# Optimization experiments

Measured on AMD Instinct MI355X. Metric: run time of the kernel, lower is better.

Reference implementation:

```python
import jax, jax.numpy as jnp
import numpy as np

IMG = 64
N = IMG * IMG          # 4096, spatial tokens = LayerNorm dim
F2 = 128 * 128         # 16384, feature_size**2 = Mlp input dim
B, C = 8, 512
EPS = 1e-5
LOG_MAX = float(np.log(1.0 / 0.01))  # clamp max for logit_scale


def setup_inputs() -> dict:
    key = jax.random.key(0)
    ks = jax.random.split(key, 8)
    s1 = 1.0 / np.sqrt(F2)
    s2 = 1.0 / np.sqrt(N)
    return {
        "x": jax.random.normal(ks[0], (B, C, N), jnp.float32),
        "feature": jax.random.normal(ks[1], (B, C, F2), jnp.float32),
        "fc1_w": jax.random.uniform(ks[2], (N, F2), jnp.float32, -s1, s1),
        "fc1_b": jax.random.uniform(ks[3], (N,), jnp.float32, -s1, s1),
        "fc2_w": jax.random.uniform(ks[4], (N, N), jnp.float32, -s2, s2),
        "fc2_b": jax.random.uniform(ks[5], (N,), jnp.float32, -s2, s2),
        "logit_scale": jnp.full((1, 1, N), np.log(10.0), jnp.float32),
        "norm_w": jnp.ones((N,), jnp.float32),
        "norm_b": jnp.zeros((N,), jnp.float32),
    }


def reference(x, feature, fc1_w, fc1_b, fc2_w, fc2_b, logit_scale, norm_w, norm_b):
    # Mlp: (B,C,F2) -> (B,C,N), ReLU activation, drop=0
    h = jax.nn.relu(jnp.einsum('bcf,nf->bcn', feature, fc1_w) + fc1_b)
    feat = jnp.einsum('bch,nh->bcn', h, fc2_w) + fc2_b        # (B,C,N)
    feat = jnp.swapaxes(feat, 1, 2)                            # (B,N,C)
    scale = jnp.exp(jnp.minimum(logit_scale, LOG_MAX))         # (1,1,N)
    temp = jnp.einsum('bnc,bcm->bnm', feat, x) * scale         # (B,N,N)
    temp = jax.nn.softmax(temp, axis=1)                        # softmax over dim=1
    out = jnp.einsum('bcn,bnm->bcm', x, temp)                  # (B,C,N)
    # LayerNorm over last dim
    mu = jnp.mean(out, axis=-1, keepdims=True)
    var = jnp.var(out, axis=-1, keepdims=True)
    out = (out - mu) * jax.lax.rsqrt(var + EPS) * norm_w + norm_b
    return out
```

## Files before the change

### kernel.cpp

```cpp
#include <hip/hip_runtime.h>
#include <stdint.h>

using u16 = unsigned short;
typedef unsigned int u32;
typedef __attribute__((ext_vector_type(4))) float f32x4;
typedef __attribute__((ext_vector_type(8))) short short8;

typedef const __attribute__((address_space(1))) u32* gas_ptr;
typedef __attribute__((address_space(3))) u32* las_ptr;

__device__ __forceinline__ u16 f2bf_u(float f) {
    u32 u = __builtin_bit_cast(u32, f);
    u32 r = 0x7fffu + ((u >> 16) & 1u);
    return (u16)((u + r) >> 16);
}
__device__ __forceinline__ float bfu2f(u16 h) {
    u32 u = ((u32)h) << 16;
    return __builtin_bit_cast(float, u);
}
__device__ __forceinline__ void split2(float v, u16& hi, u16& lo) {
    hi = f2bf_u(v);
    lo = f2bf_u(v - bfu2f(hi));
}

__device__ __forceinline__ void gload16(const void* g, void* l) {
    __builtin_amdgcn_global_load_lds((gas_ptr)g, (las_ptr)l, 16, 0, 0);
}


#define STAGE(CBUF, KT)                                                      \
  {                                                                          \
    const int kk_ = (KT) << 5;                                               \
    _Pragma("unroll")                                                        \
    for (int it_ = 0; it_ < 2; ++it_) {                                      \
      const int rb_ = it_ * 128 + w * 16;                                    \
      const int lo_ = (CBUF) * 8192 + rb_ * 32;                              \
      const size_t ga_ = (size_t)(brow + rb_ + srow) * lda + (kk_ + sca);    \
      const size_t gb_ = (size_t)(bcol + rb_ + srow) * lda + (kk_ + sca);    \
      gload16(A0 + ga_, &As0[lo_]);                                          \
      gload16(B0 + gb_, &Bs0[lo_]);                                          \
      if constexpr (SPLIT) gload16(A1 + ga_, &As1[lo_]);                     \
    }                                                                        \
  }

#define BLOQ(Q, KT)                                                          \
  {                                                                          \
    const u16* bb_ = B1 + (size_t)(bcol + wc * 64 + lr) * lda                \
                     + (((KT) << 5) + ((l >> 4) * 8));                       \
    _Pragma("unroll")                                                        \
    for (int n_ = 0; n_ < 4; ++n_)                                           \
      Q[n_] = *(const short8*)(bb_ + (size_t)(n_ * 16) * lda);               \
  }

#define AREAD(DSTH, DSTL, I)                                                 \
  {                                                                          \
    const int ro_ = cbv_ * 8192 +                                            \
        (lrw + (((I) >> 2) * 64 + ((I) & 3) * 16)) * 32 + cr;                \
    DSTH = *(const short8*)&As0[ro_];                                        \
    if constexpr (SPLIT) DSTL = *(const short8*)&As1[ro_];                   \
  }

#define PHASE(KT, CB, Q)                                                     \
  {                                                                          \
    const int cbv_ = (CB);                                                   \
    if ((KT) == NT - 1) {                                                    \
      asm volatile("s_waitcnt vmcnt(0)" ::: "memory");                       \
    } else {                                                                 \
      if constexpr (SPLIT) asm volatile("s_waitcnt vmcnt(10)" ::: "memory"); \
      else asm volatile("s_waitcnt vmcnt(4)" ::: "memory");                  \
    }                                                                        \
    __builtin_amdgcn_s_barrier();                                            \
    __builtin_amdgcn_sched_barrier(0);                                       \
    {                                                                        \
      int cs_ = cbv_ + 2; if (cs_ >= 3) cs_ -= 3;                            \
      if ((KT) + 2 < NT) STAGE(cs_, (KT) + 2);                               \
    }                                                                        \
    short8 bh_[4];                                                           \
    _Pragma("unroll")                                                        \
    for (int n_ = 0; n_ < 4; ++n_)                                           \
      bh_[n_] = *(const short8*)&Bs0[cbv_ * 8192 +                           \
                                     (wc * 64 + n_ * 16 + lr) * 32 + cr];    \
    short8 ah_[2][2], al_[2][2];                                             \
    AREAD(ah_[0][0], al_[0][0], 0);                                          \
    AREAD(ah_[0][1], al_[0][1], 1);                                          \
    __builtin_amdgcn_sched_barrier(0);                                       \
    _Pragma("unroll")                                                        \
    for (int j_ = 0; j_ < 4; ++j_) {                                         \
      const int p_ = j_ & 1;                                                 \
      if (j_ < 3) {                                                          \
        AREAD(ah_[p_ ^ 1][0], al_[p_ ^ 1][0], 2 * j_ + 2);                   \
        AREAD(ah_[p_ ^ 1][1], al_[p_ ^ 1][1], 2 * j_ + 3);                   \
      }                                                                      \
      __builtin_amdgcn_sched_barrier(0);                                     \
      __builtin_amdgcn_s_setprio(1);                                         \
      _Pragma("unroll")                                                      \
      for (int ii_ = 0; ii_ < 2; ++ii_) {                                    \
        const int i_ = 2 * j_ + ii_;                                         \
        _Pragma("unroll")                                                    \
        for (int n_ = 0; n_ < 4; ++n_)                                       \
          acc[i_][n_] = __builtin_amdgcn_mfma_f32_16x16x32_bf16(             \
              ah_[p_][ii_], bh_[n_], acc[i_][n_], 0, 0, 0);                  \
        if constexpr (SPLIT) {                                               \
          _Pragma("unroll")                                                  \
          for (int n_ = 0; n_ < 4; ++n_)                                     \
            acc[i_][n_] = __builtin_amdgcn_mfma_f32_16x16x32_bf16(           \
                al_[p_][ii_], bh_[n_], acc[i_][n_], 0, 0, 0);                \
          _Pragma("unroll")                                                  \
          for (int n_ = 0; n_ < 4; ++n_)                                     \
            acc[i_][n_] = __builtin_amdgcn_mfma_f32_16x16x32_bf16(           \
                ah_[p_][ii_], Q[n_], acc[i_][n_], 0, 0, 0);                  \
        }                                                                    \
      }                                                                      \
      __builtin_amdgcn_s_setprio(0);                                         \
    }                                                                        \
    __builtin_amdgcn_sched_barrier(0);                                       \
    if ((KT) + 2 < NT) { if constexpr (SPLIT) BLOQ(Q, (KT) + 2); }           \
    __builtin_amdgcn_sched_barrier(0);                                       \
  }

template<int EPI, bool SPLIT>
__global__ __launch_bounds__(512, 2)
void gemm256(const u16* __restrict__ Ah, const u16* __restrict__ Al,
             const u16* __restrict__ Bh, const u16* __restrict__ Bl,
             int K, int lda, int N,
             const float* __restrict__ aux,
             void* __restrict__ out0, void* __restrict__ out1,
             size_t strideA, size_t strideB, size_t strideO)
{
    extern __shared__ __align__(16) u16 lds[];
    u16* const As0 = lds;
    u16* const Bs0 = lds + 3 * 8192;
    u16* const As1 = SPLIT ? (lds + 6 * 8192) : lds;

    const int t = threadIdx.x;
    const int w = t >> 6;
    const int l = t & 63;

    int brow, bcol;
    const int gx = gridDim.x, gy = gridDim.y;
    const int orig = blockIdx.y * gx + blockIdx.x;
    if (gx == 16 && gy == 16) {
        const int x = orig & 7, j = orig >> 3;
        brow = ((x & 3) * 4 + (j & 3)) * 256;
        bcol = ((x >> 2) * 8 + (j >> 2)) * 256;
    } else {
        const int nwg = gx * gy;
        const int swz = (orig & 7) * (nwg >> 3) + (orig >> 3);
        brow = (swz / gx) * 256;
        bcol = (swz % gx) * 256;
    }
    const int z = blockIdx.z;

    const u16* A0 = Ah + (size_t)z * strideA;
    const u16* A1 = SPLIT ? (Al + (size_t)z * strideA) : nullptr;
    const u16* B0 = Bh + (size_t)z * strideB;
    const u16* B1 = SPLIT ? (Bl + (size_t)z * strideB) : nullptr;

    const int srow = l >> 2;
    const int sca = ((l & 3) ^ ((l >> 3) & 3)) * 8;

    const int wr = w >> 2;
    const int wc = w & 3;
    const int lr = l & 15;
    const int cr = ((l >> 4) ^ ((l >> 1) & 3)) * 8;
    const int lrw = wr * 128 + lr;

    f32x4 acc[8][4];
    const f32x4 zero = {0.f, 0.f, 0.f, 0.f};
#pragma unroll
    for (int i = 0; i < 8; ++i)
#pragma unroll
        for (int j = 0; j < 4; ++j) acc[i][j] = zero;

    const int NT = K >> 5;
    short8 qA[4], qB[4];

    STAGE(0, 0);
    if constexpr (SPLIT) BLOQ(qA, 0);
    STAGE(1, 1);
    if constexpr (SPLIT) BLOQ(qB, 1);
    if constexpr (SPLIT)
        asm volatile("s_waitcnt vmcnt(10)" ::: "memory");
    else
        asm volatile("s_waitcnt vmcnt(4)" ::: "memory");
    __builtin_amdgcn_s_barrier();
    __builtin_amdgcn_sched_barrier(0);

    int cb = 0;
    for (int kt = 0; kt < NT; kt += 2) {
        PHASE(kt, cb, qA);
        cb = (cb == 2) ? 0 : cb + 1;
        PHASE(kt + 1, cb, qB);
        cb = (cb == 2) ? 0 : cb + 1;
    }

#pragma unroll
    for (int mh = 0; mh < 2; ++mh)
#pragma unroll
        for (int m = 0; m < 4; ++m)
#pragma unroll
            for (int n = 0; n < 4; ++n)
#pragma unroll
                for (int j = 0; j < 4; ++j) {
                    const int row = brow + wr * 128 + mh * 64 + m * 16 + (l >> 4) * 4 + j;
                    const int col = bcol + wc * 64 + n * 16 + (l & 15);
                    float v = acc[mh * 4 + m][n][j];
                    if (EPI == 0) {
                        v += aux[col];
                        v = fmaxf(v, 0.f);
                        u16 hi, lo; split2(v, hi, lo);
                        ((u16*)out0)[(size_t)row * N + col] = hi;
                        ((u16*)out1)[(size_t)row * N + col] = lo;
                    } else if (EPI == 1) {
                        v += aux[col];
                        const int bb = row >> 9, cc = row & 511;
                        const size_t idx = ((size_t)bb * N + col) * 512 + cc;
                        u16 hi, lo; split2(v, hi, lo);
                        ((u16*)out0)[idx] = hi;
                        ((u16*)out1)[idx] = lo;
                    } else if (EPI == 2) {
                        ((float*)out0)[(size_t)row * N + col] = v;
                    } else {
                        ((float*)out0)[(size_t)z * strideO + (size_t)row * N + col] = v;
                    }
                }
}

__global__ void split_k(const float* __restrict__ in, u16* __restrict__ hi,
                        u16* __restrict__ lo, size_t n4)
{
    size_t i = blockIdx.x * (size_t)blockDim.x + threadIdx.x;
    const size_t stride = (size_t)gridDim.x * blockDim.x;
    for (; i < n4; i += stride) {
        const float4 v = ((const float4*)in)[i];
        ushort4 h, l;
        split2(v.x, h.x, l.x);
        split2(v.y, h.y, l.y);
        split2(v.z, h.z, l.z);
        split2(v.w, h.w, l.w);
        ((ushort4*)hi)[i] = h;
        ((ushort4*)lo)[i] = l;
    }
}

__global__ void conv_bf16_k(const float* __restrict__ in, u16* __restrict__ out, size_t n4)
{
    size_t i = blockIdx.x * (size_t)blockDim.x + threadIdx.x;
    const size_t stride = (size_t)gridDim.x * blockDim.x;
    for (; i < n4; i += stride) {
        const float4 v = ((const float4*)in)[i];
        ushort4 o;
        o.x = f2bf_u(v.x); o.y = f2bf_u(v.y); o.z = f2bf_u(v.z); o.w = f2bf_u(v.w);
        ((ushort4*)out)[i] = o;
    }
}

__global__ void transpose_split_x(const float* __restrict__ x,
                                  u16* __restrict__ xt_hi, u16* __restrict__ xt_lo)
{
    __shared__ float tile[32][33];
    const int b = blockIdx.z;
    const int n0 = blockIdx.x * 32;
    const int c0 = blockIdx.y * 32;
    const int tx = threadIdx.x, ty = threadIdx.y;
#pragma unroll
    for (int k = 0; k < 4; ++k)
        tile[ty + 8 * k][tx] = x[((size_t)b * 512 + c0 + ty + 8 * k) * 4096 + n0 + tx];
    __syncthreads();
#pragma unroll
    for (int k = 0; k < 4; ++k) {
        const float v = tile[tx][ty + 8 * k];
        u16 hi, lo; split2(v, hi, lo);
        const size_t idx = ((size_t)b * 4096 + n0 + ty + 8 * k) * 512 + c0 + tx;
        xt_hi[idx] = hi;
        xt_lo[idx] = lo;
    }
}

__global__ void scale_prep(const float* __restrict__ ls, float* __restrict__ s)
{
    const int i = blockIdx.x * blockDim.x + threadIdx.x;
    if (i < 4096) s[i] = expf(fminf(ls[i], 4.605170185988092f));
}

__global__ __launch_bounds__(256)
void softmax_rows(const float* __restrict__ T, const float* __restrict__ s, u16* __restrict__ P)
{
    const int m = blockIdx.x;
    const int t = threadIdx.x;
    const float sc = s[m];
    const float* row = T + (size_t)m * 4096;
    float v[16];
    float mx = -3.402823e38f;
#pragma unroll
    for (int i = 0; i < 16; ++i) {
        v[i] = row[t + 256 * i] * sc;
        mx = fmaxf(mx, v[i]);
    }
#pragma unroll
    for (int o = 32; o; o >>= 1) mx = fmaxf(mx, __shfl_xor(mx, o, 64));
    __shared__ float sm[4], ss[4];
    if ((t & 63) == 0) sm[t >> 6] = mx;
    __syncthreads();
    mx = fmaxf(fmaxf(sm[0], sm[1]), fmaxf(sm[2], sm[3]));
    float sum = 0.f;
#pragma unroll
    for (int i = 0; i < 16; ++i) {
        v[i] = expf(v[i] - mx);
        sum += v[i];
    }
#pragma unroll
    for (int o = 32; o; o >>= 1) sum += __shfl_xor(sum, o, 64);
    if ((t & 63) == 0) ss[t >> 6] = sum;
    __syncthreads();
    sum = (ss[0] + ss[1]) + (ss[2] + ss[3]);
    const float inv = 1.f / sum;
#pragma unroll
    for (int i = 0; i < 16; ++i)
        P[(size_t)m * 4096 + t + 256 * i] = f2bf_u(v[i] * inv);
}

__global__ __launch_bounds__(256)
void ln_rows(const float* __restrict__ X, const float* __restrict__ gw,
             const float* __restrict__ gb, float* __restrict__ out)
{
    const int r = blockIdx.x;
    const int t = threadIdx.x;
    const float* row = X + (size_t)r * 4096;
    float v[16];
    float s1 = 0.f, s2 = 0.f;
#pragma unroll
    for (int i = 0; i < 16; ++i) {
        v[i] = row[t + 256 * i];
        s1 += v[i];
        s2 += v[i] * v[i];
    }
#pragma unroll
    for (int o = 32; o; o >>= 1) {
        s1 += __shfl_xor(s1, o, 64);
        s2 += __shfl_xor(s2, o, 64);
    }
    __shared__ float m1[4], m2[4];
    if ((t & 63) == 0) { m1[t >> 6] = s1; m2[t >> 6] = s2; }
    __syncthreads();
    s1 = (m1[0] + m1[1]) + (m1[2] + m1[3]);
    s2 = (m2[0] + m2[1]) + (m2[2] + m2[3]);
    const float mu = s1 * (1.f / 4096.f);
    const float var = s2 * (1.f / 4096.f) - mu * mu;
    const float rs = rsqrtf(var + 1e-5f);
#pragma unroll
    for (int i = 0; i < 16; ++i) {
        const int n = t + 256 * i;
        out[(size_t)r * 4096 + n] = (v[i] - mu) * rs * gw[n] + gb[n];
    }
}

extern "C" void kernel_launch(void* const* d_in, const int* in_sizes, int n_in,
                              void* d_out, int out_size, void* d_ws, size_t ws_size,
                              hipStream_t stream)
{
    const float* x  = (const float*)d_in[0];
    const float* fe = (const float*)d_in[1];
    const float* w1 = (const float*)d_in[2];
    const float* b1 = (const float*)d_in[3];
    const float* w2 = (const float*)d_in[4];
    const float* b2 = (const float*)d_in[5];
    const float* ls = (const float*)d_in[6];
    const float* nw = (const float*)d_in[7];
    const float* nb = (const float*)d_in[8];
    float* out = (float*)d_out;
    char* ws = (char*)d_ws;

    if (ws_size < 637550592ull) return;

    hipFuncSetAttribute((const void*)gemm256<0, true>,
                        hipFuncAttributeMaxDynamicSharedMemorySize, 147456);
    hipFuncSetAttribute((const void*)gemm256<1, true>,
                        hipFuncAttributeMaxDynamicSharedMemorySize, 147456);
    hipFuncSetAttribute((const void*)gemm256<2, true>,
                        hipFuncAttributeMaxDynamicSharedMemorySize, 147456);
    hipFuncSetAttribute((const void*)gemm256<3, false>,
                        hipFuncAttributeMaxDynamicSharedMemorySize, 98304);

    u16*  fhi  = (u16*) (ws + 0ull);
    u16*  flo  = (u16*) (ws + 134217728ull);
    u16*  w1hi = (u16*) (ws + 268435456ull);
    u16*  w1lo = (u16*) (ws + 402653184ull);
    u16*  hhi  = (u16*) (ws + 536870912ull);
    u16*  hlo  = (u16*) (ws + 570425344ull);
    u16*  w2hi = (u16*) (ws + 0ull);
    u16*  w2lo = (u16*) (ws + 33554432ull);
    u16*  fthi = (u16*) (ws + 67108864ull);
    u16*  ftlo = (u16*) (ws + 100663296ull);
    u16*  xthi = (u16*) (ws + 134217728ull);
    u16*  xtlo = (u16*) (ws + 167772160ull);
    u16*  xbf  = (u16*) (ws + 201326592ull);
    float* tt  = (float*)(ws + 234881024ull);
    u16*  pall = (u16*) (ws + 301989888ull);
    float* pre = (float*)(ws + 570425344ull);
    float* sv  = (float*)(ws + 637534208ull);

    split_k<<<2048, 256, 0, stream>>>(fe, fhi, flo, (size_t)16777216);
    split_k<<<2048, 256, 0, stream>>>(w1, w1hi, w1lo, (size_t)16777216);

    gemm256<0, true><<<dim3(16, 16, 1), 512, 147456, stream>>>(
        fhi, flo, w1hi, w1lo, 16384, 16384, 4096, b1, hhi, hlo, 0, 0, 0);

    split_k<<<2048, 256, 0, stream>>>(w2, w2hi, w2lo, (size_t)4194304);

    gemm256<1, true><<<dim3(16, 16, 1), 512, 147456, stream>>>(
        hhi, hlo, w2hi, w2lo, 4096, 4096, 4096, b2, fthi, ftlo, 0, 0, 0);

    transpose_split_x<<<dim3(128, 16, 8), dim3(32, 8), 0, stream>>>(x, xthi, xtlo);
    conv_bf16_k<<<2048, 256, 0, stream>>>(x, xbf, (size_t)4194304);
    scale_prep<<<16, 256, 0, stream>>>(ls, sv);

    for (int b = 0; b < 8; ++b) {
        const size_t o = (size_t)b * 4096 * 512;
        gemm256<2, true><<<dim3(16, 16, 1), 512, 147456, stream>>>(
            xthi + o, xtlo + o, fthi + o, ftlo + o, 512, 512, 4096,
            nullptr, tt, nullptr, 0, 0, 0);
        softmax_rows<<<4096, 256, 0, stream>>>(tt, sv, pall + (size_t)b * 16777216);
    }

    gemm256<3, false><<<dim3(16, 2, 8), 512, 98304, stream>>>(
        xbf, nullptr, pall, nullptr, 4096, 4096, 4096, nullptr, pre, nullptr,
        (size_t)512 * 4096, (size_t)4096 * 4096, (size_t)512 * 4096);

    ln_rows<<<4096, 256, 0, stream>>>(pre, nw, nb, out);
}
```

Before: 2.722 ms.

## Restructure split-bf16 GEMM main loop into four fenced sub-phases with interleaved staging

For the split (hi/lo) GEMM path, each K-tile is now processed in four quadrant sub-phases, each with its own barriers. The global-to-LDS stage loads for A-hi, B and A-lo are spread across those sub-phases, and the vmcnt wait moves to the end of the tile. The aim is to interleave memory issue with MFMA bursts and keep the A fragments resident across two quadrants, in the style of a ping-pong schedule. The non-split path is simplified to read one A fragment at a time. The extra barriers per tile add synchronisation overhead, and the changed wait counts risk reading data that has not landed yet.

Measured after the change: 2.766 ms. About the same (+1.6%).

```diff
diff --git a/kernel.cpp b/kernel.cpp
--- a/kernel.cpp
+++ b/kernel.cpp
@@ -26,6 +26,8 @@
 __device__ __forceinline__ void gload16(const void* g, void* l) {
     __builtin_amdgcn_global_load_lds((gas_ptr)g, (las_ptr)l, 16, 0, 0);
 }
+
+#define MFMA16(A, B, C) __builtin_amdgcn_mfma_f32_16x16x32_bf16((A), (B), (C), 0, 0, 0)
 
 
 #define STAGE(CBUF, KT)                                                      \
@@ -43,6 +45,17 @@
     }                                                                        \
   }
 
+#define STAGEP(CBUF, KT, SRC, DSTARR, BASE)                                  \
+  {                                                                          \
+    const int kk_ = (KT) << 5;                                               \
+    _Pragma("unroll")                                                        \
+    for (int it_ = 0; it_ < 2; ++it_) {                                      \
+      const int rb_ = it_ * 128 + w * 16;                                    \
+      gload16((SRC) + (size_t)((BASE) + rb_ + srow) * lda + (kk_ + sca),     \
+              &(DSTARR)[(CBUF) * 8192 + rb_ * 32]);                          \
+    }                                                                        \
+  }
+
 #define BLOQ(Q, KT)                                                          \
   {                                                                          \
     const u16* bb_ = B1 + (size_t)(bcol + wc * 64 + lr) * lda                \
@@ -52,22 +65,97 @@
       Q[n_] = *(const short8*)(bb_ + (size_t)(n_ * 16) * lda);               \
   }
 
-#define AREAD(DSTH, DSTL, I)                                                 \
+#define FENCE_IN                                                             \
+    __builtin_amdgcn_sched_barrier(0);                                       \
+    __builtin_amdgcn_s_barrier();                                            \
+    asm volatile("s_waitcnt lgkmcnt(0)" ::: "memory");                       \
+    __builtin_amdgcn_sched_barrier(0);
+
+#define FENCE_OUT                                                            \
+    __builtin_amdgcn_sched_barrier(0);                                       \
+    __builtin_amdgcn_s_barrier();                                            \
+    __builtin_amdgcn_sched_barrier(0);
+
+#define QUAD(AH, AL, NB, AB, Q)                                              \
+    __builtin_amdgcn_s_setprio(1);                                           \
+    _Pragma("unroll")                                                        \
+    for (int m_ = 0; m_ < 4; ++m_)                                           \
+      _Pragma("unroll")                                                      \
+      for (int n_ = 0; n_ < 2; ++n_)                                         \
+        acc[(AB) + m_][(NB) + n_] =                                          \
+            MFMA16(AH[m_], bh_[(NB) + n_], acc[(AB) + m_][(NB) + n_]);       \
+    _Pragma("unroll")                                                        \
+    for (int m_ = 0; m_ < 4; ++m_)                                           \
+      _Pragma("unroll")                                                      \
+      for (int n_ = 0; n_ < 2; ++n_)                                         \
+        acc[(AB) + m_][(NB) + n_] =                                          \
+            MFMA16(AL[m_], bh_[(NB) + n_], acc[(AB) + m_][(NB) + n_]);       \
+    _Pragma("unroll")                                                        \
+    for (int m_ = 0; m_ < 4; ++m_)                                           \
+      _Pragma("unroll")                                                      \
+      for (int n_ = 0; n_ < 2; ++n_)                                         \
+        acc[(AB) + m_][(NB) + n_] =                                          \
+            MFMA16(AH[m_], Q[(NB) + n_], acc[(AB) + m_][(NB) + n_]);         \
+    __builtin_amdgcn_s_setprio(0);
+
+#define PHASE4(KT, CB, Q)                                                    \
   {                                                                          \
-    const int ro_ = cbv_ * 8192 +                                            \
-        (lrw + (((I) >> 2) * 64 + ((I) & 3) * 16)) * 32 + cr;                \
-    DSTH = *(const short8*)&As0[ro_];                                        \
-    if constexpr (SPLIT) DSTL = *(const short8*)&As1[ro_];                   \
+    const int cbv_ = (CB);                                                   \
+    int cs_ = cbv_ + 2; if (cs_ >= 3) cs_ -= 3;                              \
+    const bool st_ = (KT) + 2 < NT;                                          \
+    short8 bh_[4], ah_[4], al_[4];                                           \
+                                               \
+    bh_[0] = *(const short8*)&Bs0[cbv_ * 8192 + (wc*64 +  0 + lr)*32 + cr];  \
+    bh_[1] = *(const short8*)&Bs0[cbv_ * 8192 + (wc*64 + 16 + lr)*32 + cr];  \
+    _Pragma("unroll")                                                        \
+    for (int m_ = 0; m_ < 4; ++m_) {                                         \
+      const int ro_ = cbv_ * 8192 + (lrw + m_ * 16) * 32 + cr;               \
+      ah_[m_] = *(const short8*)&As0[ro_];                                   \
+      al_[m_] = *(const short8*)&As1[ro_];                                   \
+    }                                                                        \
+    if (st_) STAGEP(cs_, (KT) + 2, A0, As0, brow);                           \
+    FENCE_IN                                                                 \
+    QUAD(ah_, al_, 0, 0, Q)                                                  \
+    FENCE_OUT                                                                \
+                                               \
+    bh_[2] = *(const short8*)&Bs0[cbv_ * 8192 + (wc*64 + 32 + lr)*32 + cr];  \
+    bh_[3] = *(const short8*)&Bs0[cbv_ * 8192 + (wc*64 + 48 + lr)*32 + cr];  \
+    if (st_) STAGEP(cs_, (KT) + 2, B0, Bs0, bcol);                           \
+    FENCE_IN                                                                 \
+    QUAD(ah_, al_, 2, 0, Q)                                                  \
+    FENCE_OUT                                                                \
+                                               \
+    _Pragma("unroll")                                                        \
+    for (int m_ = 0; m_ < 4; ++m_) {                                         \
+      const int ro_ = cbv_ * 8192 + (lrw + 64 + m_ * 16) * 32 + cr;          \
+      ah_[m_] = *(const short8*)&As0[ro_];                                   \
+      al_[m_] = *(const short8*)&As1[ro_];                                   \
+    }                                                                        \
+    if (st_) STAGEP(cs_, (KT) + 2, A1, As1, brow);                           \
+    FENCE_IN                                                                 \
+    QUAD(ah_, al_, 0, 4, Q)                                                  \
+    FENCE_OUT                                                                \
+    \
+    FENCE_IN                                                                 \
+    QUAD(ah_, al_, 2, 4, Q)                                                  \
+    __builtin_amdgcn_sched_barrier(0);                                       \
+    if (st_) BLOQ(Q, (KT) + 2);                                              \
+    __builtin_amdgcn_sched_barrier(0);                                       \
+    if ((KT) + 2 < NT)                                                       \
+      asm volatile("s_waitcnt vmcnt(14)" ::: "memory");                      \
+    else if ((KT) + 1 < NT)                                                  \
+      asm volatile("s_waitcnt vmcnt(4)" ::: "memory");                       \
+    __builtin_amdgcn_s_barrier();                                            \
+    __builtin_amdgcn_sched_barrier(0);                                       \
   }
 
-#define PHASE(KT, CB, Q)                                                     \
+#define PHASE1(KT, CB)                                                       \
   {                                                                          \
     const int cbv_ = (CB);                                                   \
     if ((KT) == NT - 1) {                                                    \
       asm volatile("s_waitcnt vmcnt(0)" ::: "memory");                       \
     } else {                                                                 \
-      if constexpr (SPLIT) asm volatile("s_waitcnt vmcnt(10)" ::: "memory"); \
-      else asm volatile("s_waitcnt vmcnt(4)" ::: "memory");                  \
+      asm volatile("s_waitcnt vmcnt(4)" ::: "memory");                       \
     }                                                                        \
     __builtin_amdgcn_s_barrier();                                            \
     __builtin_amdgcn_sched_barrier(0);                                       \
@@ -80,42 +168,18 @@
     for (int n_ = 0; n_ < 4; ++n_)                                           \
       bh_[n_] = *(const short8*)&Bs0[cbv_ * 8192 +                           \
                                      (wc * 64 + n_ * 16 + lr) * 32 + cr];    \
-    short8 ah_[2][2], al_[2][2];                                             \
-    AREAD(ah_[0][0], al_[0][0], 0);                                          \
-    AREAD(ah_[0][1], al_[0][1], 1);                                          \
-    __builtin_amdgcn_sched_barrier(0);                                       \
-    _Pragma("unroll")                                                        \
-    for (int j_ = 0; j_ < 4; ++j_) {                                         \
-      const int p_ = j_ & 1;                                                 \
-      if (j_ < 3) {                                                          \
-        AREAD(ah_[p_ ^ 1][0], al_[p_ ^ 1][0], 2 * j_ + 2);                   \
-        AREAD(ah_[p_ ^ 1][1], al_[p_ ^ 1][1], 2 * j_ + 3);                   \
-      }                                                                      \
-      __builtin_amdgcn_sched_barrier(0);                                     \
+    _Pragma("unroll")                                                        \
+    for (int i_ = 0; i_ < 8; ++i_) {                                         \
+      short8 ah_;                                                            \
+      const int ro_ = cbv_ * 8192 +                                          \
+          (lrw + ((i_ >> 2) * 64 + (i_ & 3) * 16)) * 32 + cr;                \
+      ah_ = *(const short8*)&As0[ro_];                                       \
       __builtin_amdgcn_s_setprio(1);                                         \
       _Pragma("unroll")                                                      \
-      for (int ii_ = 0; ii_ < 2; ++ii_) {                                    \
-        const int i_ = 2 * j_ + ii_;                                         \
-        _Pragma("unroll")                                                    \
-        for (int n_ = 0; n_ < 4; ++n_)                                       \
-          acc[i_][n_] = __builtin_amdgcn_mfma_f32_16x16x32_bf16(             \
-              ah_[p_][ii_], bh_[n_], acc[i_][n_], 0, 0, 0);                  \
-        if constexpr (SPLIT) {                                               \
-          _Pragma("unroll")                                                  \
-          for (int n_ = 0; n_ < 4; ++n_)                                     \
-            acc[i_][n_] = __builtin_amdgcn_mfma_f32_16x16x32_bf16(           \
-                al_[p_][ii_], bh_[n_], acc[i_][n_], 0, 0, 0);                \
-          _Pragma("unroll")                                                  \
-          for (int n_ = 0; n_ < 4; ++n_)                                     \
-            acc[i_][n_] = __builtin_amdgcn_mfma_f32_16x16x32_bf16(           \
-                ah_[p_][ii_], Q[n_], acc[i_][n_], 0, 0, 0);                  \
-        }                                                                    \
-      }                                                                      \
+      for (int n_ = 0; n_ < 4; ++n_)                                         \
+        acc[i_][n_] = MFMA16(ah_, bh_[n_], acc[i_][n_]);                     \
       __builtin_amdgcn_s_setprio(0);                                         \
     }                                                                        \
-    __builtin_amdgcn_sched_barrier(0);                                       \
-    if ((KT) + 2 < NT) { if constexpr (SPLIT) BLOQ(Q, (KT) + 2); }           \
-    __builtin_amdgcn_sched_barrier(0);                                       \
   }
 
 template<int EPI, bool SPLIT>
@@ -188,10 +252,17 @@
 
     int cb = 0;
     for (int kt = 0; kt < NT; kt += 2) {
-        PHASE(kt, cb, qA);
-        cb = (cb == 2) ? 0 : cb + 1;
-        PHASE(kt + 1, cb, qB);
-        cb = (cb == 2) ? 0 : cb + 1;
+        if constexpr (SPLIT) {
+            PHASE4(kt, cb, qA);
+            cb = (cb == 2) ? 0 : cb + 1;
+            PHASE4(kt + 1, cb, qB);
+            cb = (cb == 2) ? 0 : cb + 1;
+        } else {
+            PHASE1(kt, cb);
+            cb = (cb == 2) ? 0 : cb + 1;
+            PHASE1(kt + 1, cb);
+            cb = (cb == 2) ? 0 : cb + 1;
+        }
     }
 
 #pragma unroll
```
